# Kernel optimization log

Hardware: AMD Instinct MI355X
Metric: run time of the kernel (lower is better)

## Reference

```python
import jax, jax.numpy as jnp
import numpy as np

B, N, C, H = 8, 1024, 512, 8
EPS = 1e-6


def setup_inputs() -> dict:
    key = jax.random.key(0)
    k0, k1, k2, k3, k4 = jax.random.split(key, 5)
    x = jax.random.normal(k0, (B, N, C), dtype=jnp.float32)
    # nonnegative random-walk visit-frequency mask stand-in
    mask = jax.random.uniform(k1, (N, N), dtype=jnp.float32)
    w_qkv = jax.random.normal(k2, (C, 3 * C), dtype=jnp.float32) * 0.02
    w_out = jax.random.normal(k3, (C, C), dtype=jnp.float32) * 0.02
    b_out = jax.random.normal(k4, (C,), dtype=jnp.float32) * 0.02
    return {"x": x, "mask": mask, "w_qkv": w_qkv, "w_out": w_out, "b_out": b_out}


def reference(x, mask, w_qkv, w_out, b_out):
    b, n, c = x.shape
    d = c // H
    qkv = x @ w_qkv                                   # [B,N,3C]
    q, k, v = jnp.split(qkv, 3, axis=-1)

    def to_heads(t):
        return t.reshape(b, n, H, d).transpose(0, 2, 1, 3)  # [B,H,N,D]

    q, k, v = to_heads(q), to_heads(k), to_heads(v)
    # positive feature map
    q = jax.nn.relu(q) + EPS
    k = jax.nn.relu(k) + EPS
    # graph diffusion: (q^T @ mask)^T == einsum over source node m
    q = q + 0.1 * jnp.einsum('bhmd,mn->bhnd', q, mask)
    k = k + 0.1 * jnp.einsum('bhmd,mn->bhnd', k, mask)
    # linear kernel scores, elementwise-masked
    kernel = jnp.einsum('bhnd,bhmd->bhnm', q, k) * mask   # [B,H,N,N]
    z = 1.0 / (kernel.sum(axis=-1, keepdims=True) + EPS)  # [B,H,N,1]
    out = jnp.einsum('bhnm,bhmd->bhnd', kernel, v) * z    # [B,H,N,D]
    out = out.transpose(0, 2, 1, 3).reshape(b, n, c)      # [B,N,C]
    return out @ w_out + b_out
```

## Files before the change

### kernel.cpp

```cpp
#include <hip/hip_runtime.h>
#include <cstddef>

#define Bsz 8
#define Nn  1024
#define Cc  512
#define Hh  8
#define Dd  64
#define EPSF 1e-6f

typedef __attribute__((ext_vector_type(8))) short short8;
typedef __attribute__((ext_vector_type(4))) float floatx4;

static __device__ __forceinline__ short f2bf(float f) {
    union { float f; unsigned u; } v; v.f = f;
    unsigned r = (v.u + 0x7FFFu + ((v.u >> 16) & 1u)) >> 16;
    return (short)r;
}
static __device__ __forceinline__ float bf2f(short s) {
    union { unsigned u; float f; } v; v.u = ((unsigned)(unsigned short)s) << 16;
    return v.f;
}

#define GLOAD_LDS16(gp, lp)                                              \
    __builtin_amdgcn_global_load_lds(                                    \
        (const __attribute__((address_space(1))) void*)(gp),             \
        (__attribute__((address_space(3))) void*)(lp), 16, 0, 0)

static __device__ __forceinline__
void stage_tile(short* __restrict__ lds, const short* __restrict__ src,
                int ldsrc, int tid, int CHUNKS, int SLOTS) {
    #pragma unroll
    for (int s = tid; s < SLOTS; s += 256) {
        int r = s / CHUNKS, cs = s % CHUNKS;
        int gc = cs ^ (r & 7);
        GLOAD_LDS16(&src[(size_t)r * ldsrc + gc * 8], &lds[s * 8]);
    }
}
static __device__ __forceinline__
short8 fragT(const short* __restrict__ lds, int CHUNKS, int r, int lc) {
    return *(const short8*)&lds[(r * CHUNKS + (lc ^ (r & 7))) * 8];
}
static __device__ __forceinline__ int swz8(int r, int c) {
    return (r * 8 + (((c) >> 3) ^ (r & 7))) * 8 + ((c) & 7);
}

__global__ __launch_bounds__(256)
void prep_all(const float* __restrict__ x, const float* __restrict__ mask,
              const float* __restrict__ wq, const float* __restrict__ wo,
              short* __restrict__ xb, short* __restrict__ Ad,
              short* __restrict__ wqT, short* __restrict__ whi,
              short* __restrict__ wlo) {
    __shared__ float t[64][65];
    const int tid = threadIdx.x;
    const int bid = blockIdx.x;

    if (bid < 2048) {
        int idx = bid * 256 + tid;
        const float* s = &x[(size_t)idx * 8];
        union { short h[8]; int4 v; } u;
        #pragma unroll
        for (int j = 0; j < 8; j++) u.h[j] = f2bf(s[j]);
        *(int4*)&xb[(size_t)idx * 8] = u.v;
        return;
    }
    if (bid < 2304) {
        int idx = bid - 2048;
        const int n0 = (idx & 15) * 64, m0 = (idx >> 4) * 64;
        #pragma unroll
        for (int i = 0; i < 4; i++) {
            int k = i * 256 + tid;
            int r = k >> 4, c4 = (k & 15) * 4;
            *(float4*)&t[r][c4] = *(const float4*)&mask[(size_t)(m0 + r) * Nn + n0 + c4];
        }
        __syncthreads();
        #pragma unroll
        for (int i = 0; i < 4; i++) {
            int k = i * 256 + tid;
            int rr = k >> 4, c4 = (k & 15) * 4;
            union { short h[4]; int2 v; } u;
            #pragma unroll
            for (int j = 0; j < 4; j++) {
                int mm = c4 + j;
                float v = 0.1f * t[mm][rr] + ((n0 + rr) == (m0 + mm) ? 1.0f : 0.0f);
                u.h[j] = f2bf(v);
            }
            *(int2*)&Ad[(size_t)(n0 + rr) * Nn + m0 + c4] = u.v;
        }
        return;
    }
    if (bid < 2496) {
        int idx = bid - 2304;
        const int n0 = (idx % 24) * 64, k0 = (idx / 24) * 64;
        #pragma unroll
        for (int i = 0; i < 4; i++) {
            int k = i * 256 + tid;
            int r = k >> 4, c4 = (k & 15) * 4;
            *(float4*)&t[r][c4] = *(const float4*)&wq[(size_t)(k0 + r) * 1536 + n0 + c4];
        }
        __syncthreads();
        #pragma unroll
        for (int i = 0; i < 4; i++) {
            int k = i * 256 + tid;
            int rr = k >> 4, c4 = (k & 15) * 4;
            union { short h[4]; int2 v; } u;
            #pragma unroll
            for (int j = 0; j < 4; j++) u.h[j] = f2bf(t[c4 + j][rr]);
            *(int2*)&wqT[(size_t)(n0 + rr) * 512 + k0 + c4] = u.v;
        }
        return;
    }
    {
        int idx = bid - 2496;
        const int n0 = (idx & 7) * 64, k0 = (idx >> 3) * 64;
        #pragma unroll
        for (int i = 0; i < 4; i++) {
            int k = i * 256 + tid;
            int r = k >> 4, c4 = (k & 15) * 4;
            *(float4*)&t[r][c4] = *(const float4*)&wo[(size_t)(k0 + r) * 512 + n0 + c4];
        }
        __syncthreads();
        #pragma unroll
        for (int i = 0; i < 4; i++) {
            int k = i * 256 + tid;
            int rr = k >> 4, c4 = (k & 15) * 4;
            union { short h[4]; int2 v; } uh, ul;
            #pragma unroll
            for (int j = 0; j < 4; j++) {
                float v = t[c4 + j][rr];
                short hi = f2bf(v);
                uh.h[j] = hi;
                ul.h[j] = f2bf(v - bf2f(hi));
            }
            *(int2*)&whi[(size_t)(n0 + rr) * 512 + k0 + c4] = uh.v;
            *(int2*)&wlo[(size_t)(n0 + rr) * 512 + k0 + c4] = ul.v;
        }
    }
}

__global__ __launch_bounds__(256)
void gemm_qkv(const short* __restrict__ xb, const short* __restrict__ wqT,
              short* __restrict__ qT, short* __restrict__ kT,
              short* __restrict__ vT) {
    __shared__ short smem[17408];
    short* As = smem;
    short* Bs = smem + 8192;

    const int tid = threadIdx.x;
    const int m0 = blockIdx.y * 128;
    const int n0 = blockIdx.x * 128;
    const int wave = tid >> 6, lane = tid & 63;
    const int quad = lane >> 4, l16 = lane & 15;
    const int wm = (wave >> 1) * 64, wn = (wave & 1) * 64;

    floatx4 acc[4][4];
    #pragma unroll
    for (int i = 0; i < 4; i++)
        #pragma unroll
        for (int j = 0; j < 4; j++) acc[i][j] = (floatx4){0.f, 0.f, 0.f, 0.f};

    const short* Ab = xb  + (size_t)m0 * 512;
    const short* Bb = wqT + (size_t)n0 * 512;

    for (int k0 = 0; k0 < 512; k0 += 64) {
        __syncthreads();
        stage_tile(As, Ab + k0, 512, tid, 8, 1024);
        stage_tile(Bs, Bb + k0, 512, tid, 8, 1024);
        __syncthreads();
        #pragma unroll
        for (int kh = 0; kh < 2; kh++) {
            short8 a[4], b[4];
            #pragma unroll
            for (int i = 0; i < 4; i++) a[i] = fragT(As, 8, wm + i * 16 + l16, kh * 4 + quad);
            #pragma unroll
            for (int i = 0; i < 4; i++) b[i] = fragT(Bs, 8, wn + i * 16 + l16, kh * 4 + quad);
            #pragma unroll
            for (int mi = 0; mi < 4; mi++)
                #pragma unroll
                for (int ni = 0; ni < 4; ni++)
                    acc[mi][ni] = __builtin_amdgcn_mfma_f32_16x16x32_bf16(
                        a[mi], b[ni], acc[mi][ni], 0, 0, 0);
        }
    }

    __syncthreads();
    short* Tt = smem;
    const int doRelu = (n0 < 1024);
    #pragma unroll
    for (int mi = 0; mi < 4; mi++)
        #pragma unroll
        for (int ni = 0; ni < 4; ni++)
            #pragma unroll
            for (int r = 0; r < 4; r++) {
                float v = acc[mi][ni][r];
                if (doRelu) v = fmaxf(v, 0.0f) + EPSF;
                int nl = wn + ni * 16 + l16;
                int ml = wm + mi * 16 + quad * 4 + r;
                Tt[nl * 136 + ml] = f2bf(v);
            }
    __syncthreads();

    const int b = m0 >> 10, m_in = m0 & 1023;
    int row = tid >> 1, half = tid & 1;
    int cg = n0 + row;
    int part = cg >> 9, ci = cg & 511;
    short* base = (part == 0) ? qT : (part == 1) ? kT : vT;
    short* dst = base + ((size_t)b * 512 + ci) * 1024 + m_in + half * 64;
    const short* srcl = &Tt[row * 136 + half * 64];
    #pragma unroll
    for (int i = 0; i < 8; i++)
        *(int4*)&dst[i * 8] = *(const int4*)&srcl[i * 8];
}

__global__ __launch_bounds__(256)
void gemm_diff(const short* __restrict__ Ad, const short* __restrict__ qT,
               const short* __restrict__ kT, short* __restrict__ qd,
               short* __restrict__ kd) {
    __shared__ short smem[16384];
    short* As = smem;
    short* Bs = smem + 8192;

    const int tid = threadIdx.x;
    const int z = blockIdx.z, b = z >> 1, part = z & 1;
    const short* BTb = (part ? kT : qT) + (size_t)b * 512 * 1024;
    short* outb = (part ? kd : qd) + (size_t)b * 1024 * 512;

    const int r0 = blockIdx.y * 128;
    const int c0 = blockIdx.x * 128;
    const int wave = tid >> 6, lane = tid & 63;
    const int quad = lane >> 4, l16 = lane & 15;
    const int wm = (wave >> 1) * 64, wn = (wave & 1) * 64;

    floatx4 acc[4][4];
    #pragma unroll
    for (int i = 0; i < 4; i++)
        #pragma unroll
        for (int j = 0; j < 4; j++) acc[i][j] = (floatx4){0.f, 0.f, 0.f, 0.f};

    const short* Ab = Ad  + (size_t)r0 * 1024;
    const short* Bb = BTb + (size_t)c0 * 1024;

    for (int k0 = 0; k0 < 1024; k0 += 64) {
        __syncthreads();
        stage_tile(As, Ab + k0, 1024, tid, 8, 1024);
        stage_tile(Bs, Bb + k0, 1024, tid, 8, 1024);
        __syncthreads();
        #pragma unroll
        for (int kh = 0; kh < 2; kh++) {
            short8 a[4], b2[4];
            #pragma unroll
            for (int i = 0; i < 4; i++) a[i]  = fragT(As, 8, wm + i * 16 + l16, kh * 4 + quad);
            #pragma unroll
            for (int i = 0; i < 4; i++) b2[i] = fragT(Bs, 8, wn + i * 16 + l16, kh * 4 + quad);
            #pragma unroll
            for (int mi = 0; mi < 4; mi++)
                #pragma unroll
                for (int ni = 0; ni < 4; ni++)
                    acc[mi][ni] = __builtin_amdgcn_mfma_f32_16x16x32_bf16(
                        a[mi], b2[ni], acc[mi][ni], 0, 0, 0);
        }
    }

    #pragma unroll
    for (int mi = 0; mi < 4; mi++)
        #pragma unroll
        for (int r = 0; r < 4; r++) {
            int n = r0 + wm + mi * 16 + quad * 4 + r;
            #pragma unroll
            for (int ni = 0; ni < 4; ni++) {
                int c = c0 + wn + ni * 16 + l16;
                outb[(size_t)n * 512 + c] = f2bf(acc[mi][ni][r]);
            }
        }
}

__global__ __launch_bounds__(256)
void attn_mfma(const short* __restrict__ qd, const short* __restrict__ kd,
               const short* __restrict__ vTg, const float* __restrict__ mask,
               short* __restrict__ ahi, short* __restrict__ alo) {
    __shared__ short qs[4096];
    __shared__ short ks[8192];
    __shared__ short vt[8192];
    __shared__ short ss[4096];

    const int tid = threadIdx.x;
    const int bh = blockIdx.y;
    const int b = bh >> 3, h = bh & 7;
    const int n0 = blockIdx.x * 64;

    const int wave = tid >> 6, lane = tid & 63;
    const int quad = lane >> 4, l16 = lane & 15;

    const short* Qb = qd + ((size_t)b * Nn + n0) * Cc + h * Dd;
    const short* Kb = kd + (size_t)b * Nn * Cc + h * Dd;
    const short* Vb = vTg + ((size_t)b * Cc + h * Dd) * Nn;
    const float* Mb = mask + (size_t)n0 * Nn;

    stage_tile(qs, Qb, Cc, tid, 8, 512);
    __syncthreads();
    const short8 a0 = fragT(qs, 8, wave * 16 + l16, quad);
    const short8 a1 = fragT(qs, 8, wave * 16 + l16, 4 + quad);

    float dreg[4] = {0.f, 0.f, 0.f, 0.f};
    floatx4 nacc[4];
    #pragma unroll
    for (int i = 0; i < 4; i++) nacc[i] = (floatx4){0.f, 0.f, 0.f, 0.f};

    for (int m0 = 0; m0 < Nn; m0 += 128) {
        __syncthreads();
        stage_tile(ks, Kb + (size_t)m0 * Cc, Cc, tid, 8, 1024);
        stage_tile(vt, Vb + m0, Nn, tid, 16, 1024);
        __syncthreads();

        #pragma unroll
        for (int half = 0; half < 2; half++) {
            const int mh = half * 64;
            #pragma unroll
            for (int mt = 0; mt < 4; mt++) {
                const short8 b0 = fragT(ks, 8, mh + mt * 16 + l16, quad);
                const short8 b1 = fragT(ks, 8, mh + mt * 16 + l16, 4 + quad);
                floatx4 s = (floatx4){0.f, 0.f, 0.f, 0.f};
                s = __builtin_amdgcn_mfma_f32_16x16x32_bf16(a0, b0, s, 0, 0, 0);
                s = __builtin_amdgcn_mfma_f32_16x16x32_bf16(a1, b1, s, 0, 0, 0);
                #pragma unroll
                for (int r = 0; r < 4; r++) {
                    int rl = wave * 16 + quad * 4 + r;
                    float mv = Mb[(size_t)rl * Nn + m0 + mh + mt * 16 + l16];
                    float sv = s[r] * mv;
                    dreg[r] += sv;
                    ss[swz8(rl, mt * 16 + l16)] = f2bf(sv);
                }
            }

            const short8 p0 = fragT(ss, 8, wave * 16 + l16, quad);
            const short8 p1 = fragT(ss, 8, wave * 16 + l16, 4 + quad);
            #pragma unroll
            for (int dt = 0; dt < 4; dt++) {
                const short8 v0 = fragT(vt, 16, dt * 16 + l16, half * 8 + quad);
                const short8 v1 = fragT(vt, 16, dt * 16 + l16, half * 8 + 4 + quad);
                nacc[dt] = __builtin_amdgcn_mfma_f32_16x16x32_bf16(p0, v0, nacc[dt], 0, 0, 0);
                nacc[dt] = __builtin_amdgcn_mfma_f32_16x16x32_bf16(p1, v1, nacc[dt], 0, 0, 0);
            }
        }
    }

    #pragma unroll
    for (int r = 0; r < 4; r++) {
        #pragma unroll
        for (int off = 1; off < 16; off <<= 1)
            dreg[r] += __shfl_xor(dreg[r], off, 64);
    }

    #pragma unroll
    for (int r = 0; r < 4; r++) {
        int n = n0 + wave * 16 + quad * 4 + r;
        float zr = 1.0f / (dreg[r] + EPSF);
        #pragma unroll
        for (int dt = 0; dt < 4; dt++) {
            float val = nacc[dt][r] * zr;
            short hi = f2bf(val);
            short lo = f2bf(val - bf2f(hi));
            size_t o = ((size_t)b * Nn + n) * Cc + h * Dd + dt * 16 + l16;
            ahi[o] = hi;
            alo[o] = lo;
        }
    }
}

__global__ __launch_bounds__(256)
void gemm_out(const short* __restrict__ ahi, const short* __restrict__ alo,
              const short* __restrict__ whi, const short* __restrict__ wlo,
              const float* __restrict__ bias, float* __restrict__ out) {
    __shared__ short smem[24576];
    short* Ah = smem;
    short* Al = smem + 4096;
    short* Bh = smem + 8192;
    short* Bl = smem + 16384;

    const int tid = threadIdx.x;
    const int m0 = blockIdx.y * 64;
    const int n0 = blockIdx.x * 128;
    const int wave = tid >> 6, lane = tid & 63;
    const int quad = lane >> 4, l16 = lane & 15;
    const int wm = (wave >> 1) * 32, wn = (wave & 1) * 64;

    floatx4 acc[2][4];
    #pragma unroll
    for (int i = 0; i < 2; i++)
        #pragma unroll
        for (int j = 0; j < 4; j++) acc[i][j] = (floatx4){0.f, 0.f, 0.f, 0.f};

    const short* Ahb = ahi + (size_t)m0 * 512;
    const short* Alb = alo + (size_t)m0 * 512;
    const short* Bhb = whi + (size_t)n0 * 512;
    const short* Blb = wlo + (size_t)n0 * 512;

    for (int k0 = 0; k0 < 512; k0 += 64) {
        __syncthreads();
        stage_tile(Ah, Ahb + k0, 512, tid, 8, 512);
        stage_tile(Al, Alb + k0, 512, tid, 8, 512);
        stage_tile(Bh, Bhb + k0, 512, tid, 8, 1024);
        stage_tile(Bl, Blb + k0, 512, tid, 8, 1024);
        __syncthreads();
        #pragma unroll
        for (int kh = 0; kh < 2; kh++) {
            short8 ah[2], al[2], bh[4], bl[4];
            #pragma unroll
            for (int i = 0; i < 2; i++) {
                ah[i] = fragT(Ah, 8, wm + i * 16 + l16, kh * 4 + quad);
                al[i] = fragT(Al, 8, wm + i * 16 + l16, kh * 4 + quad);
            }
            #pragma unroll
            for (int i = 0; i < 4; i++) {
                bh[i] = fragT(Bh, 8, wn + i * 16 + l16, kh * 4 + quad);
                bl[i] = fragT(Bl, 8, wn + i * 16 + l16, kh * 4 + quad);
            }
            #pragma unroll
            for (int mi = 0; mi < 2; mi++)
                #pragma unroll
                for (int ni = 0; ni < 4; ni++) {
                    acc[mi][ni] = __builtin_amdgcn_mfma_f32_16x16x32_bf16(
                        ah[mi], bh[ni], acc[mi][ni], 0, 0, 0);
                    acc[mi][ni] = __builtin_amdgcn_mfma_f32_16x16x32_bf16(
                        ah[mi], bl[ni], acc[mi][ni], 0, 0, 0);
                    acc[mi][ni] = __builtin_amdgcn_mfma_f32_16x16x32_bf16(
                        al[mi], bh[ni], acc[mi][ni], 0, 0, 0);
                }
        }
    }

    #pragma unroll
    for (int mi = 0; mi < 2; mi++)
        #pragma unroll
        for (int r = 0; r < 4; r++) {
            int m = m0 + wm + mi * 16 + quad * 4 + r;
            #pragma unroll
            for (int ni = 0; ni < 4; ni++) {
                int n = n0 + wn + ni * 16 + l16;
                out[(size_t)m * 512 + n] = acc[mi][ni][r] + bias[n];
            }
        }
}

extern "C" void kernel_launch(void* const* d_in, const int* in_sizes, int n_in,
                              void* d_out, int out_size, void* d_ws, size_t ws_size,
                              hipStream_t stream) {
    const float* x     = (const float*)d_in[0];
    const float* mask  = (const float*)d_in[1];
    const float* w_qkv = (const float*)d_in[2];
    const float* w_out = (const float*)d_in[3];
    const float* b_out = (const float*)d_in[4];
    float* out = (float*)d_out;

    char* p = (char*)d_ws;
    short* xb  = (short*)p; p += 8388608;
    short* wqT = (short*)p; p += 1572864;
    short* Ad  = (short*)p; p += 2097152;
    short* whi = (short*)p; p += 524288;
    short* wlo = (short*)p; p += 524288;
    short* qT  = (short*)p; p += 8388608;
    short* kT  = (short*)p; p += 8388608;
    short* vT  = (short*)p; p += 8388608;
    short* qd  = (short*)p; p += 8388608;
    short* kd  = (short*)p; p += 8388608;
    short* ahi = (short*)p; p += 8388608;
    short* alo = (short*)p; p += 8388608;

    dim3 blk(256);

    prep_all  <<<2560, blk, 0, stream>>>(x, mask, w_qkv, w_out,
                                         xb, Ad, wqT, whi, wlo);
    gemm_qkv  <<<dim3(12, 64), blk, 0, stream>>>(xb, wqT, qT, kT, vT);
    gemm_diff <<<dim3(4, 8, 16), blk, 0, stream>>>(Ad, qT, kT, qd, kd);
    attn_mfma <<<dim3(16, 64), blk, 0, stream>>>(qd, kd, vT, mask, ahi, alo);
    gemm_out  <<<dim3(4, 128), blk, 0, stream>>>(ahi, alo, whi, wlo, b_out, out);
}
```

Before: 188.2 us.

## Retile attention kernel to 128 query rows per block with 64-key chunks

The attention kernel now processes 128 query rows per block, with each wave owning two 16-row tiles, and iterates over keys in 64-wide chunks. Each staged K/V tile and its fragments are reused across twice as many query rows, which halves global K/V traffic and LDS fragment reads per output. In exchange the grid is halved to 512 blocks, register pressure rises from the doubled accumulators, and there are twice as many synchronisation steps per row.

```diff
diff --git a/kernel.cpp b/kernel.cpp
--- a/kernel.cpp
+++ b/kernel.cpp
@@ -277,15 +277,15 @@
 void attn_mfma(const short* __restrict__ qd, const short* __restrict__ kd,
                const short* __restrict__ vTg, const float* __restrict__ mask,
                short* __restrict__ ahi, short* __restrict__ alo) {
-    __shared__ short qs[4096];
-    __shared__ short ks[8192];
-    __shared__ short vt[8192];
-    __shared__ short ss[4096];
+    __shared__ short qs[8192];
+    __shared__ short ks[4096];
+    __shared__ short vt[4096];
+    __shared__ short ss[8192];
 
     const int tid = threadIdx.x;
     const int bh = blockIdx.y;
     const int b = bh >> 3, h = bh & 7;
-    const int n0 = blockIdx.x * 64;
+    const int n0 = blockIdx.x * 128;
 
     const int wave = tid >> 6, lane = tid & 63;
     const int quad = lane >> 4, l16 = lane & 15;
@@ -295,75 +295,91 @@
     const short* Vb = vTg + ((size_t)b * Cc + h * Dd) * Nn;
     const float* Mb = mask + (size_t)n0 * Nn;
 
-    stage_tile(qs, Qb, Cc, tid, 8, 512);
+    stage_tile(qs, Qb, Cc, tid, 8, 1024);
     __syncthreads();
-    const short8 a0 = fragT(qs, 8, wave * 16 + l16, quad);
-    const short8 a1 = fragT(qs, 8, wave * 16 + l16, 4 + quad);
-
-    float dreg[4] = {0.f, 0.f, 0.f, 0.f};
-    floatx4 nacc[4];
-    #pragma unroll
-    for (int i = 0; i < 4; i++) nacc[i] = (floatx4){0.f, 0.f, 0.f, 0.f};
-
-    for (int m0 = 0; m0 < Nn; m0 += 128) {
-        __syncthreads();
-        stage_tile(ks, Kb + (size_t)m0 * Cc, Cc, tid, 8, 1024);
-        stage_tile(vt, Vb + m0, Nn, tid, 16, 1024);
-        __syncthreads();
-
-        #pragma unroll
-        for (int half = 0; half < 2; half++) {
-            const int mh = half * 64;
-            #pragma unroll
-            for (int mt = 0; mt < 4; mt++) {
-                const short8 b0 = fragT(ks, 8, mh + mt * 16 + l16, quad);
-                const short8 b1 = fragT(ks, 8, mh + mt * 16 + l16, 4 + quad);
+    short8 aT[2][2];
+    #pragma unroll
+    for (int t = 0; t < 2; t++) {
+        aT[t][0] = fragT(qs, 8, wave * 32 + t * 16 + l16, quad);
+        aT[t][1] = fragT(qs, 8, wave * 32 + t * 16 + l16, 4 + quad);
+    }
+
+    float dreg[2][4] = {};
+    floatx4 nacc[2][4];
+    #pragma unroll
+    for (int t = 0; t < 2; t++)
+        #pragma unroll
+        for (int i = 0; i < 4; i++) nacc[t][i] = (floatx4){0.f, 0.f, 0.f, 0.f};
+
+    for (int m0 = 0; m0 < Nn; m0 += 64) {
+        __syncthreads();
+        stage_tile(ks, Kb + (size_t)m0 * Cc, Cc, tid, 8, 512);
+        stage_tile(vt, Vb + m0, Nn, tid, 8, 512);
+        __syncthreads();
+
+        #pragma unroll
+        for (int mt = 0; mt < 4; mt++) {
+            const short8 b0 = fragT(ks, 8, mt * 16 + l16, quad);
+            const short8 b1 = fragT(ks, 8, mt * 16 + l16, 4 + quad);
+            #pragma unroll
+            for (int t = 0; t < 2; t++) {
                 floatx4 s = (floatx4){0.f, 0.f, 0.f, 0.f};
-                s = __builtin_amdgcn_mfma_f32_16x16x32_bf16(a0, b0, s, 0, 0, 0);
-                s = __builtin_amdgcn_mfma_f32_16x16x32_bf16(a1, b1, s, 0, 0, 0);
+                s = __builtin_amdgcn_mfma_f32_16x16x32_bf16(aT[t][0], b0, s, 0, 0, 0);
+                s = __builtin_amdgcn_mfma_f32_16x16x32_bf16(aT[t][1], b1, s, 0, 0, 0);
                 #pragma unroll
                 for (int r = 0; r < 4; r++) {
-                    int rl = wave * 16 + quad * 4 + r;
-                    float mv = Mb[(size_t)rl * Nn + m0 + mh + mt * 16 + l16];
+                    int rl = wave * 32 + t * 16 + quad * 4 + r;
+                    float mv = Mb[(size_t)rl * Nn + m0 + mt * 16 + l16];
                     float sv = s[r] * mv;
-                    dreg[r] += sv;
+                    dreg[t][r] += sv;
                     ss[swz8(rl, mt * 16 + l16)] = f2bf(sv);
                 }
             }
-
-            const short8 p0 = fragT(ss, 8, wave * 16 + l16, quad);
-            const short8 p1 = fragT(ss, 8, wave * 16 + l16, 4 + quad);
+        }
+
+        short8 p[2][2];
+        #pragma unroll
+        for (int t = 0; t < 2; t++) {
+            p[t][0] = fragT(ss, 8, wave * 32 + t * 16 + l16, quad);
+            p[t][1] = fragT(ss, 8, wave * 32 + t * 16 + l16, 4 + quad);
+        }
+        #pragma unroll
+        for (int dt = 0; dt < 4; dt++) {
+            const short8 v0 = fragT(vt, 8, dt * 16 + l16, quad);
+            const short8 v1 = fragT(vt, 8, dt * 16 + l16, 4 + quad);
+            #pragma unroll
+            for (int t = 0; t < 2; t++) {
+                nacc[t][dt] = __builtin_amdgcn_mfma_f32_16x16x32_bf16(p[t][0], v0, nacc[t][dt], 0, 0, 0);
+                nacc[t][dt] = __builtin_amdgcn_mfma_f32_16x16x32_bf16(p[t][1], v1, nacc[t][dt], 0, 0, 0);
+            }
+        }
+    }
+
+    #pragma unroll
+    for (int t = 0; t < 2; t++)
+        #pragma unroll
+        for (int r = 0; r < 4; r++) {
+            #pragma unroll
+            for (int off = 1; off < 16; off <<= 1)
+                dreg[t][r] += __shfl_xor(dreg[t][r], off, 64);
+        }
+
+    #pragma unroll
+    for (int t = 0; t < 2; t++)
+        #pragma unroll
+        for (int r = 0; r < 4; r++) {
+            int n = n0 + wave * 32 + t * 16 + quad * 4 + r;
+            float zr = 1.0f / (dreg[t][r] + EPSF);
             #pragma unroll
             for (int dt = 0; dt < 4; dt++) {
-                const short8 v0 = fragT(vt, 16, dt * 16 + l16, half * 8 + quad);
-                const short8 v1 = fragT(vt, 16, dt * 16 + l16, half * 8 + 4 + quad);
-                nacc[dt] = __builtin_amdgcn_mfma_f32_16x16x32_bf16(p0, v0, nacc[dt], 0, 0, 0);
-                nacc[dt] = __builtin_amdgcn_mfma_f32_16x16x32_bf16(p1, v1, nacc[dt], 0, 0, 0);
-            }
-        }
-    }
-
-    #pragma unroll
-    for (int r = 0; r < 4; r++) {
-        #pragma unroll
-        for (int off = 1; off < 16; off <<= 1)
-            dreg[r] += __shfl_xor(dreg[r], off, 64);
-    }
-
-    #pragma unroll
-    for (int r = 0; r < 4; r++) {
-        int n = n0 + wave * 16 + quad * 4 + r;
-        float zr = 1.0f / (dreg[r] + EPSF);
-        #pragma unroll
-        for (int dt = 0; dt < 4; dt++) {
-            float val = nacc[dt][r] * zr;
-            short hi = f2bf(val);
-            short lo = f2bf(val - bf2f(hi));
-            size_t o = ((size_t)b * Nn + n) * Cc + h * Dd + dt * 16 + l16;
-            ahi[o] = hi;
-            alo[o] = lo;
-        }
-    }
+                float val = nacc[t][dt][r] * zr;
+                short hi = f2bf(val);
+                short lo = f2bf(val - bf2f(hi));
+                size_t o = ((size_t)b * Nn + n) * Cc + h * Dd + dt * 16 + l16;
+                ahi[o] = hi;
+                alo[o] = lo;
+            }
+        }
 }
 
 __global__ __launch_bounds__(256)
@@ -471,6 +487,6 @@
                                          xb, Ad, wqT, whi, wlo);
     gemm_qkv  <<<dim3(12, 64), blk, 0, stream>>>(xb, wqT, qT, kT, vT);
     gemm_diff <<<dim3(4, 8, 16), blk, 0, stream>>>(Ad, qT, kT, qd, kd);
-    attn_mfma <<<dim3(16, 64), blk, 0, stream>>>(qd, kd, vT, mask, ahi, alo);
+    attn_mfma <<<dim3(8, 64),  blk, 0, stream>>>(qd, kd, vT, mask, ahi, alo);
     gemm_out  <<<dim3(4, 128), blk, 0, stream>>>(ahi, alo, whi, wlo, b_out, out);
 }
```

New measurement: 184.8 us. No clear change (-1.8%).
